# Performance work log

Measured on AMD Instinct MI355X. Metric: run time of the kernel, lower is better.

The kernel has to match this reference:

```python
import jax, jax.numpy as jnp
import numpy as np

H = 64  # hidden_size hardcoded in the module


def _lstm_scan(x_pre, w_hh):
    # x_pre: [T, B, 4H] = x @ W_ih^T + b_ih + b_hh, precomputed for all steps
    # w_hh: [4H, H]. PyTorch gate order: i, f, g, o.
    B = x_pre.shape[1]
    h0 = jnp.zeros((B, H), x_pre.dtype)
    c0 = jnp.zeros((B, H), x_pre.dtype)

    def cell(carry, xp):
        h, c = carry
        gates = xp + h @ w_hh.T  # [B, 4H]
        i, f, g, o = jnp.split(gates, 4, axis=-1)
        i = jax.nn.sigmoid(i)
        f = jax.nn.sigmoid(f)
        g = jnp.tanh(g)
        o = jax.nn.sigmoid(o)
        c = f * c + i * g
        h = o * jnp.tanh(c)
        return (h, c), h

    _, hs = jax.lax.scan(cell, (h0, c0), x_pre)
    return hs  # [T, B, H]


def _bidir_layer(x, w_ih, w_hh, b_ih, b_hh):
    # x: [T, B, D]; w_ih: [2, 4H, D]; w_hh: [2, 4H, H]; b_*: [2, 4H]
    pre_f = jnp.einsum('tbd,gd->tbg', x, w_ih[0]) + b_ih[0] + b_hh[0]
    hs_f = _lstm_scan(pre_f, w_hh[0])
    xr = x[::-1]
    pre_b = jnp.einsum('tbd,gd->tbg', xr, w_ih[1]) + b_ih[1] + b_hh[1]
    hs_b = _lstm_scan(pre_b, w_hh[1])[::-1]  # re-reverse to align with time
    return jnp.concatenate([hs_f, hs_b], axis=-1)  # [T, B, 2H]


def setup_inputs() -> dict:
    key = jax.random.key(0)
    B, T, F = 1024, 512, 32
    ks = jax.random.split(key, 11)
    s = 1.0 / float(np.sqrt(H))  # PyTorch LSTM init: U(-1/sqrt(H), 1/sqrt(H))
    u = lambda k, shape: jax.random.uniform(k, shape, jnp.float32, -s, s)
    return dict(
        x=jax.random.normal(ks[0], (B, T, F), jnp.float32),
        w_ih0=u(ks[1], (2, 4 * H, F)),
        w_hh0=u(ks[2], (2, 4 * H, H)),
        b_ih0=u(ks[3], (2, 4 * H)),
        b_hh0=u(ks[4], (2, 4 * H)),
        w_ih1=u(ks[5], (2, 4 * H, 2 * H)),
        w_hh1=u(ks[6], (2, 4 * H, H)),
        b_ih1=u(ks[7], (2, 4 * H)),
        b_hh1=u(ks[8], (2, 4 * H)),
        fc_w=u(ks[9], (2, 2 * H)),
        fc_b=u(ks[10], (2,)),
    )


def reference(x, w_ih0, w_hh0, b_ih0, b_hh0, w_ih1, w_hh1, b_ih1, b_hh1, fc_w, fc_b):
    xt = jnp.transpose(x, (1, 0, 2))  # [T, B, F]
    h1 = _bidir_layer(xt, w_ih0, w_hh0, b_ih0, b_hh0)  # [T, B, 2H]
    h2 = _bidir_layer(h1, w_ih1, w_hh1, b_ih1, b_hh1)  # [T, B, 2H]
    last = h2[-1]  # out[:, -1, :] in batch_first layout -> [B, 2H]
    return last @ fc_w.T + fc_b  # [B, 2]
```

## Files before the change

kernel.cpp:

```cpp
#include <hip/hip_runtime.h>

#define TT 512
#define BB 1024
#define FF 32
#define HH 64
#define GG 256

__device__ float g_h1[(size_t)TT * BB * 2 * HH];
__device__ float g_pre0[(size_t)2 * TT * BB * GG];
__device__ float g_pre1[(size_t)TT * BB * GG];
__device__ float g_hf[(size_t)BB * HH];

__device__ __forceinline__ float fsigm(float x) {
    float e = __builtin_amdgcn_exp2f(x * -1.44269504088896f);
    return __builtin_amdgcn_rcpf(1.0f + e);
}
__device__ __forceinline__ float ftanh(float x) {
    float e = __builtin_amdgcn_exp2f(x * -2.88539008177793f);
    return 2.0f * __builtin_amdgcn_rcpf(1.0f + e) - 1.0f;
}
__device__ __forceinline__ float rlane(float v, int l) {
    return __int_as_float(__builtin_amdgcn_readlane(__float_as_int(v), l));
}

#define FMA4(c, s, b) do { c.x += (s)*(b).x; c.y += (s)*(b).y; \
                           c.z += (s)*(b).z; c.w += (s)*(b).w; } while (0)

__global__ __launch_bounds__(256, 4) void pre_gemm0(
    const float* __restrict__ x,
    const float* __restrict__ w_ih,
    const float* __restrict__ b_ih,
    const float* __restrict__ b_hh)
{
    __shared__ __align__(16) float As[64 * 36];
    __shared__ __align__(16) float Bs[32 * 68];

    const int tid   = threadIdx.x;
    const int dir   = (int)(blockIdx.x >> 15);
    const int rem   = (int)(blockIdx.x & 32767);
    const int mt    = rem >> 2;
    const int n0    = (rem & 3) * 64;
    const int mbase = mt << 6;
    const int t     = mbase >> 10;
    const int b0    = mbase & 1023;

#pragma unroll
    for (int i = 0; i < 2; ++i) {
        const int qid = tid + 256 * i;
        const int r = qid >> 3, q = qid & 7;
        float4 v = *(const float4*)(x + ((size_t)(b0 + r) * TT + t) * FF + q * 4);
        *(float4*)(&As[r * 36 + q * 4]) = v;
    }
#pragma unroll
    for (int i = 0; i < 2; ++i) {
        const int qid = tid + 256 * i;
        const int r = qid >> 3, q = qid & 7;
        float4 v = *(const float4*)(w_ih + ((size_t)dir * GG + n0 + r) * FF + q * 4);
        Bs[(q * 4 + 0) * 68 + r] = v.x;
        Bs[(q * 4 + 1) * 68 + r] = v.y;
        Bs[(q * 4 + 2) * 68 + r] = v.z;
        Bs[(q * 4 + 3) * 68 + r] = v.w;
    }
    __syncthreads();

    const int tx = tid & 15, ty = tid >> 4;

    float4 c0 = make_float4(0.f, 0.f, 0.f, 0.f);
    float4 c1 = c0, c2 = c0, c3 = c0;

#pragma unroll
    for (int kq = 0; kq < 8; ++kq) {
        const float4 a0 = *(const float4*)&As[(ty * 4 + 0) * 36 + kq * 4];
        const float4 a1 = *(const float4*)&As[(ty * 4 + 1) * 36 + kq * 4];
        const float4 a2 = *(const float4*)&As[(ty * 4 + 2) * 36 + kq * 4];
        const float4 a3 = *(const float4*)&As[(ty * 4 + 3) * 36 + kq * 4];
        const float4 b0_ = *(const float4*)&Bs[(kq * 4 + 0) * 68 + tx * 4];
        const float4 b1_ = *(const float4*)&Bs[(kq * 4 + 1) * 68 + tx * 4];
        const float4 b2_ = *(const float4*)&Bs[(kq * 4 + 2) * 68 + tx * 4];
        const float4 b3_ = *(const float4*)&Bs[(kq * 4 + 3) * 68 + tx * 4];
        FMA4(c0, a0.x, b0_); FMA4(c0, a0.y, b1_); FMA4(c0, a0.z, b2_); FMA4(c0, a0.w, b3_);
        FMA4(c1, a1.x, b0_); FMA4(c1, a1.y, b1_); FMA4(c1, a1.z, b2_); FMA4(c1, a1.w, b3_);
        FMA4(c2, a2.x, b0_); FMA4(c2, a2.y, b1_); FMA4(c2, a2.z, b2_); FMA4(c2, a2.w, b3_);
        FMA4(c3, a3.x, b0_); FMA4(c3, a3.y, b1_); FMA4(c3, a3.z, b2_); FMA4(c3, a3.w, b3_);
    }

    float4 bias4;
    {
        const int g = dir * GG + n0 + tx * 4;
        bias4.x = b_ih[g + 0] + b_hh[g + 0];
        bias4.y = b_ih[g + 1] + b_hh[g + 1];
        bias4.z = b_ih[g + 2] + b_hh[g + 2];
        bias4.w = b_ih[g + 3] + b_hh[g + 3];
    }
    FMA4(c0, 1.f, bias4); FMA4(c1, 1.f, bias4);
    FMA4(c2, 1.f, bias4); FMA4(c3, 1.f, bias4);

    float* ob = g_pre0 +
        (((size_t)dir * TT + t) * BB + (b0 + ty * 4)) * GG + n0 + tx * 4;
    *(float4*)(ob + 0 * (size_t)GG) = c0;
    *(float4*)(ob + 1 * (size_t)GG) = c1;
    *(float4*)(ob + 2 * (size_t)GG) = c2;
    *(float4*)(ob + 3 * (size_t)GG) = c3;
}

#define PINQ(wq) \
    asm volatile("" : "+v"(wq.x), "+v"(wq.y), "+v"(wq.z), "+v"(wq.w))

template <int L>
__global__ __launch_bounds__(64, 1) void lstm_scan(
    const float* __restrict__ w_hh)
{
    const int l   = threadIdx.x;
    const int dir = (L == 0) ? (blockIdx.x & 1) : 0;
    const int b   = (L == 0) ? (int)(blockIdx.x >> 1) : (int)blockIdx.x;

    const float* wbase = w_hh + (size_t)dir * GG * HH;

    const float4* pi_ = (const float4*)(wbase + (size_t)(0  + l) * HH);
    const float4* pf_ = (const float4*)(wbase + (size_t)(64 + l) * HH);
    float4 wi0 = pi_[0],  wi1 = pi_[1],  wi2 = pi_[2],  wi3 = pi_[3],
           wi4 = pi_[4],  wi5 = pi_[5],  wi6 = pi_[6],  wi7 = pi_[7],
           wi8 = pi_[8],  wi9 = pi_[9],  wi10 = pi_[10], wi11 = pi_[11],
           wi12 = pi_[12], wi13 = pi_[13], wi14 = pi_[14], wi15 = pi_[15];
    float4 wf0 = pf_[0],  wf1 = pf_[1],  wf2 = pf_[2],  wf3 = pf_[3],
           wf4 = pf_[4],  wf5 = pf_[5],  wf6 = pf_[6],  wf7 = pf_[7],
           wf8 = pf_[8],  wf9 = pf_[9],  wf10 = pf_[10], wf11 = pf_[11],
           wf12 = pf_[12], wf13 = pf_[13], wf14 = pf_[14], wf15 = pf_[15];
    PINQ(wi0);  PINQ(wi1);  PINQ(wi2);  PINQ(wi3);
    PINQ(wi4);  PINQ(wi5);  PINQ(wi6);  PINQ(wi7);
    PINQ(wi8);  PINQ(wi9);  PINQ(wi10); PINQ(wi11);
    PINQ(wi12); PINQ(wi13); PINQ(wi14); PINQ(wi15);
    PINQ(wf0);  PINQ(wf1);  PINQ(wf2);  PINQ(wf3);
    PINQ(wf4);  PINQ(wf5);  PINQ(wf6);  PINQ(wf7);
    PINQ(wf8);  PINQ(wf9);  PINQ(wf10); PINQ(wf11);
    PINQ(wf12); PINQ(wf13); PINQ(wf14); PINQ(wf15);

    float4 wg[16], wo[16];
    {
        const float4* pg_ = (const float4*)(wbase + (size_t)(128 + l) * HH);
        const float4* po_ = (const float4*)(wbase + (size_t)(192 + l) * HH);
#pragma unroll
        for (int q = 0; q < 16; ++q) { wg[q] = pg_[q]; wo[q] = po_[q]; }
    }

    const float* pre = (L == 0) ? (g_pre0 + (size_t)dir * TT * BB * GG) : g_pre1;

    float c = 0.f, h = 0.f;

    const int t0 = dir ? (TT - 1) : 0;
    const int t1 = dir ? (TT - 2) : 1;
    const float* pp0 = pre + ((size_t)t0 * BB + b) * GG;
    const float* pp1 = pre + ((size_t)t1 * BB + b) * GG;
    float ci0 = pp0[l], cf0 = pp0[64 + l], cg0 = pp0[128 + l], co0 = pp0[192 + l];
    float ci1 = pp1[l], cf1 = pp1[64 + l], cg1 = pp1[128 + l], co1 = pp1[192 + l];

    for (int s = 0; s < TT; ++s) {
        const int t = dir ? (TT - 1 - s) : s;

        float ni = 0.f, nf = 0.f, ng = 0.f, no_ = 0.f;
        if (s + 2 < TT) {
            const int tn = dir ? (TT - 3 - s) : (s + 2);
            const float* np = pre + ((size_t)tn * BB + b) * GG;
            ni = np[l]; nf = np[64 + l]; ng = np[128 + l]; no_ = np[192 + l];
        }

        float ai = ci0, af = cf0, ag = cg0, ao = co0;

#define STEPQ(q) do {                                                        \
        float s0 = rlane(h, 4*q+0), s1 = rlane(h, 4*q+1),                    \
              s2 = rlane(h, 4*q+2), s3 = rlane(h, 4*q+3);                    \
        ai += s0*wi##q.x + s1*wi##q.y + s2*wi##q.z + s3*wi##q.w;             \
        af += s0*wf##q.x + s1*wf##q.y + s2*wf##q.z + s3*wf##q.w;             \
        ag += s0*wg[q].x + s1*wg[q].y + s2*wg[q].z + s3*wg[q].w;             \
        ao += s0*wo[q].x + s1*wo[q].y + s2*wo[q].z + s3*wo[q].w;             \
    } while (0)

        STEPQ(0);  STEPQ(1);  STEPQ(2);  STEPQ(3);
        STEPQ(4);  STEPQ(5);  STEPQ(6);  STEPQ(7);
        STEPQ(8);  STEPQ(9);  STEPQ(10); STEPQ(11);
        STEPQ(12); STEPQ(13); STEPQ(14); STEPQ(15);
#undef STEPQ

        const float ig = fsigm(ai);
        const float fg = fsigm(af);
        const float gg = ftanh(ag);
        const float og = fsigm(ao);
        c = fg * c + ig * gg;
        h = og * ftanh(c);

        if (L == 0) {
            g_h1[((size_t)t * BB + b) * (2 * HH) + dir * HH + l] = h;
        } else {
            if (s == TT - 1) g_hf[(size_t)b * HH + l] = h;
        }

        ci0 = ci1; cf0 = cf1; cg0 = cg1; co0 = co1;
        ci1 = ni;  cf1 = nf;  cg1 = ng;  co1 = no_;
    }
}

__global__ __launch_bounds__(256, 2) void pre_gemm1(
    const float* __restrict__ w_ih,
    const float* __restrict__ b_ih,
    const float* __restrict__ b_hh)
{
    __shared__ __align__(16) float As[64 * 132];
    __shared__ __align__(16) float Bs[128 * 68];

    const int tid   = threadIdx.x;
    const int mbase = (int)(blockIdx.x >> 2) * 64;
    const int n0    = (int)(blockIdx.x & 3) * 64;

#pragma unroll
    for (int i = 0; i < 8; ++i) {
        const int qid = tid + 256 * i;
        const int r = qid >> 5, q = qid & 31;
        float4 v = *(const float4*)(g_h1 + (size_t)(mbase + r) * 128 + q * 4);
        *(float4*)(&As[r * 132 + q * 4]) = v;
    }
#pragma unroll
    for (int i = 0; i < 8; ++i) {
        const int qid = tid + 256 * i;
        const int r = qid >> 5, q = qid & 31;
        float4 v = *(const float4*)(w_ih + (size_t)(n0 + r) * 128 + q * 4);
        Bs[(q * 4 + 0) * 68 + r] = v.x;
        Bs[(q * 4 + 1) * 68 + r] = v.y;
        Bs[(q * 4 + 2) * 68 + r] = v.z;
        Bs[(q * 4 + 3) * 68 + r] = v.w;
    }
    __syncthreads();

    const int tx = tid & 15, ty = tid >> 4;

    float4 c0 = make_float4(0.f, 0.f, 0.f, 0.f);
    float4 c1 = c0, c2 = c0, c3 = c0;

#pragma unroll 8
    for (int kq = 0; kq < 32; ++kq) {
        const float4 a0 = *(const float4*)&As[(ty * 4 + 0) * 132 + kq * 4];
        const float4 a1 = *(const float4*)&As[(ty * 4 + 1) * 132 + kq * 4];
        const float4 a2 = *(const float4*)&As[(ty * 4 + 2) * 132 + kq * 4];
        const float4 a3 = *(const float4*)&As[(ty * 4 + 3) * 132 + kq * 4];
        const float4 b0 = *(const float4*)&Bs[(kq * 4 + 0) * 68 + tx * 4];
        const float4 b1 = *(const float4*)&Bs[(kq * 4 + 1) * 68 + tx * 4];
        const float4 b2 = *(const float4*)&Bs[(kq * 4 + 2) * 68 + tx * 4];
        const float4 b3 = *(const float4*)&Bs[(kq * 4 + 3) * 68 + tx * 4];
        FMA4(c0, a0.x, b0); FMA4(c0, a0.y, b1); FMA4(c0, a0.z, b2); FMA4(c0, a0.w, b3);
        FMA4(c1, a1.x, b0); FMA4(c1, a1.y, b1); FMA4(c1, a1.z, b2); FMA4(c1, a1.w, b3);
        FMA4(c2, a2.x, b0); FMA4(c2, a2.y, b1); FMA4(c2, a2.z, b2); FMA4(c2, a2.w, b3);
        FMA4(c3, a3.x, b0); FMA4(c3, a3.y, b1); FMA4(c3, a3.z, b2); FMA4(c3, a3.w, b3);
    }

    float4 bias4;
    bias4.x = b_ih[n0 + tx * 4 + 0] + b_hh[n0 + tx * 4 + 0];
    bias4.y = b_ih[n0 + tx * 4 + 1] + b_hh[n0 + tx * 4 + 1];
    bias4.z = b_ih[n0 + tx * 4 + 2] + b_hh[n0 + tx * 4 + 2];
    bias4.w = b_ih[n0 + tx * 4 + 3] + b_hh[n0 + tx * 4 + 3];

    FMA4(c0, 1.f, bias4); FMA4(c1, 1.f, bias4);
    FMA4(c2, 1.f, bias4); FMA4(c3, 1.f, bias4);

    float* ob = g_pre1 + (size_t)(mbase + ty * 4) * GG + n0 + tx * 4;
    *(float4*)(ob + 0 * (size_t)GG) = c0;
    *(float4*)(ob + 1 * (size_t)GG) = c1;
    *(float4*)(ob + 2 * (size_t)GG) = c2;
    *(float4*)(ob + 3 * (size_t)GG) = c3;
}

#define FMAC4(W, P0, P1, P2, P3, K) do{                                   \
    float4 v_;                                                           \
    v_ = (P0)[K]; acc0 += W.x*v_.x; acc0 += W.y*v_.y; acc0 += W.z*v_.z; acc0 += W.w*v_.w; \
    v_ = (P1)[K]; acc1 += W.x*v_.x; acc1 += W.y*v_.y; acc1 += W.z*v_.z; acc1 += W.w*v_.w; \
    v_ = (P2)[K]; acc2 += W.x*v_.x; acc2 += W.y*v_.y; acc2 += W.z*v_.z; acc2 += W.w*v_.w; \
    v_ = (P3)[K]; acc3 += W.x*v_.x; acc3 += W.y*v_.y; acc3 += W.z*v_.z; acc3 += W.w*v_.w; \
}while(0)

__global__ __launch_bounds__(256, 2) void lstm_final(
    const float* __restrict__ w_ih,
    const float* __restrict__ b_ih,
    const float* __restrict__ b_hh,
    const float* __restrict__ fc_w,
    const float* __restrict__ fc_b,
    float* __restrict__ out)
{
    const int tid = threadIdx.x;
    const int b0  = blockIdx.x * 4;

    __shared__ __align__(16) float x_lds[4][128];
    __shared__ __align__(16) float gact[4][GG];
    __shared__ __align__(16) float last[4][128];

#pragma unroll
    for (int r = 0; r < 2; ++r) {
        int idx = tid + r * 256;
        int b = idx >> 7, col = idx & 127;
        x_lds[b][col] = g_h1[((size_t)(TT - 1) * BB + (b0 + b)) * 128 + col];
    }

    const float4* p = (const float4*)(w_ih + ((size_t)GG + tid) * 128);
    float4 w0 = p[0],  w1 = p[1],  w2 = p[2],  w3 = p[3],  w4 = p[4],  w5 = p[5],
           w6 = p[6],  w7 = p[7],  w8 = p[8],  w9 = p[9],  w10 = p[10], w11 = p[11],
           w12 = p[12], w13 = p[13], w14 = p[14], w15 = p[15], w16 = p[16], w17 = p[17],
           w18 = p[18], w19 = p[19], w20 = p[20], w21 = p[21], w22 = p[22], w23 = p[23],
           w24 = p[24], w25 = p[25], w26 = p[26], w27 = p[27], w28 = p[28], w29 = p[29],
           w30 = p[30], w31 = p[31];
    const float bias = b_ih[GG + tid] + b_hh[GG + tid];
    __syncthreads();

    const float4* xb0 = (const float4*)x_lds[0];
    const float4* xb1 = (const float4*)x_lds[1];
    const float4* xb2 = (const float4*)x_lds[2];
    const float4* xb3 = (const float4*)x_lds[3];

    float acc0 = bias, acc1 = bias, acc2 = bias, acc3 = bias;
    FMAC4(w0, xb0, xb1, xb2, xb3, 0);   FMAC4(w1, xb0, xb1, xb2, xb3, 1);
    FMAC4(w2, xb0, xb1, xb2, xb3, 2);   FMAC4(w3, xb0, xb1, xb2, xb3, 3);
    FMAC4(w4, xb0, xb1, xb2, xb3, 4);   FMAC4(w5, xb0, xb1, xb2, xb3, 5);
    FMAC4(w6, xb0, xb1, xb2, xb3, 6);   FMAC4(w7, xb0, xb1, xb2, xb3, 7);
    FMAC4(w8, xb0, xb1, xb2, xb3, 8);   FMAC4(w9, xb0, xb1, xb2, xb3, 9);
    FMAC4(w10, xb0, xb1, xb2, xb3, 10); FMAC4(w11, xb0, xb1, xb2, xb3, 11);
    FMAC4(w12, xb0, xb1, xb2, xb3, 12); FMAC4(w13, xb0, xb1, xb2, xb3, 13);
    FMAC4(w14, xb0, xb1, xb2, xb3, 14); FMAC4(w15, xb0, xb1, xb2, xb3, 15);
    FMAC4(w16, xb0, xb1, xb2, xb3, 16); FMAC4(w17, xb0, xb1, xb2, xb3, 17);
    FMAC4(w18, xb0, xb1, xb2, xb3, 18); FMAC4(w19, xb0, xb1, xb2, xb3, 19);
    FMAC4(w20, xb0, xb1, xb2, xb3, 20); FMAC4(w21, xb0, xb1, xb2, xb3, 21);
    FMAC4(w22, xb0, xb1, xb2, xb3, 22); FMAC4(w23, xb0, xb1, xb2, xb3, 23);
    FMAC4(w24, xb0, xb1, xb2, xb3, 24); FMAC4(w25, xb0, xb1, xb2, xb3, 25);
    FMAC4(w26, xb0, xb1, xb2, xb3, 26); FMAC4(w27, xb0, xb1, xb2, xb3, 27);
    FMAC4(w28, xb0, xb1, xb2, xb3, 28); FMAC4(w29, xb0, xb1, xb2, xb3, 29);
    FMAC4(w30, xb0, xb1, xb2, xb3, 30); FMAC4(w31, xb0, xb1, xb2, xb3, 31);

    const bool is_g = ((tid >> 6) == 2);
    gact[0][tid] = is_g ? ftanh(acc0) : fsigm(acc0);
    gact[1][tid] = is_g ? ftanh(acc1) : fsigm(acc1);
    gact[2][tid] = is_g ? ftanh(acc2) : fsigm(acc2);
    gact[3][tid] = is_g ? ftanh(acc3) : fsigm(acc3);
    __syncthreads();

    {
        const int cb = tid >> 6, cj = tid & 63;
        float ig = gact[cb][cj];
        float gg = gact[cb][2 * HH + cj];
        float og = gact[cb][3 * HH + cj];
        float c = ig * gg;
        float h = og * ftanh(c);
        last[cb][HH + cj] = h;
        last[cb][cj] = g_hf[(size_t)(b0 + cb) * HH + cj];
    }
    __syncthreads();

    if (tid < 8) {
        int b = tid >> 1, o = tid & 1;
        float a = fc_b[o];
#pragma unroll
        for (int j = 0; j < 128; ++j) a += fc_w[o * 128 + j] * last[b][j];
        out[(size_t)(b0 + b) * 2 + o] = a;
    }
}

extern "C" void kernel_launch(void* const* d_in, const int* in_sizes, int n_in,
                              void* d_out, int out_size, void* d_ws, size_t ws_size,
                              hipStream_t stream) {
    const float* x     = (const float*)d_in[0];
    const float* w_ih0 = (const float*)d_in[1];
    const float* w_hh0 = (const float*)d_in[2];
    const float* b_ih0 = (const float*)d_in[3];
    const float* b_hh0 = (const float*)d_in[4];
    const float* w_ih1 = (const float*)d_in[5];
    const float* w_hh1 = (const float*)d_in[6];
    const float* b_ih1 = (const float*)d_in[7];
    const float* b_hh1 = (const float*)d_in[8];
    const float* fc_w  = (const float*)d_in[9];
    const float* fc_b  = (const float*)d_in[10];
    float* out = (float*)d_out;

    pre_gemm0<<<65536, 256, 0, stream>>>(x, w_ih0, b_ih0, b_hh0);
    lstm_scan<0><<<2048, 64, 0, stream>>>(w_hh0);
    pre_gemm1<<<32768, 256, 0, stream>>>(w_ih1, b_ih1, b_hh1);
    lstm_scan<1><<<1024, 64, 0, stream>>>(w_hh1);
    lstm_final<<<256, 256, 0, stream>>>(w_ih1, b_ih1, b_hh1, fc_w, fc_b, out);
}
```

Measured before the change: 2.570 ms.

## Switch pre-activation and layer-1 hidden buffers from time-major to batch-major layout

Reorders g_pre0, g_pre1 and g_h1 from [T][B] to [B][T] indexing. The first-layer GEMM now tiles along time within one batch row, and each scan block streams its pre-activations from one contiguous region instead of jumping 1 MB per step. The goal is better DRAM/TLB locality and prefetching for the latency-bound recurrent loop. The trade-off is that per-step h1 writes across blocks are now strided in memory, and any hidden kernel that assumes time-major rows must stay consistent.

Measured after the change: 2.687 ms. 4.5% more time.

```diff
diff --git a/kernel.cpp b/kernel.cpp
--- a/kernel.cpp
+++ b/kernel.cpp
@@ -6,9 +6,9 @@
 #define HH 64
 #define GG 256
 
-__device__ float g_h1[(size_t)TT * BB * 2 * HH];
-__device__ float g_pre0[(size_t)2 * TT * BB * GG];
-__device__ float g_pre1[(size_t)TT * BB * GG];
+__device__ float g_h1[(size_t)BB * TT * 2 * HH];
+__device__ float g_pre0[(size_t)2 * BB * TT * GG];
+__device__ float g_pre1[(size_t)BB * TT * GG];
 __device__ float g_hf[(size_t)BB * HH];
 
 __device__ __forceinline__ float fsigm(float x) {
@@ -36,19 +36,19 @@
     __shared__ __align__(16) float Bs[32 * 68];
 
     const int tid   = threadIdx.x;
-    const int dir   = (int)(blockIdx.x >> 15);
-    const int rem   = (int)(blockIdx.x & 32767);
-    const int mt    = rem >> 2;
+    const int bid   = (int)blockIdx.x;
+    const int dir   = bid >> 15;
+    const int rem   = bid & 32767;
+    const int mtile = rem >> 2;
     const int n0    = (rem & 3) * 64;
-    const int mbase = mt << 6;
-    const int t     = mbase >> 10;
-    const int b0    = mbase & 1023;
+    const int b     = mtile >> 3;
+    const int t0    = (mtile & 7) << 6;
 
 #pragma unroll
     for (int i = 0; i < 2; ++i) {
         const int qid = tid + 256 * i;
         const int r = qid >> 3, q = qid & 7;
-        float4 v = *(const float4*)(x + ((size_t)(b0 + r) * TT + t) * FF + q * 4);
+        float4 v = *(const float4*)(x + ((size_t)b * TT + t0 + r) * FF + q * 4);
         *(float4*)(&As[r * 36 + q * 4]) = v;
     }
 #pragma unroll
@@ -96,7 +96,7 @@
     FMA4(c2, 1.f, bias4); FMA4(c3, 1.f, bias4);
 
     float* ob = g_pre0 +
-        (((size_t)dir * TT + t) * BB + (b0 + ty * 4)) * GG + n0 + tx * 4;
+        (((size_t)dir * BB + b) * TT + (t0 + ty * 4)) * GG + n0 + tx * 4;
     *(float4*)(ob + 0 * (size_t)GG) = c0;
     *(float4*)(ob + 1 * (size_t)GG) = c1;
     *(float4*)(ob + 2 * (size_t)GG) = c2;
@@ -143,14 +143,16 @@
         for (int q = 0; q < 16; ++q) { wg[q] = pg_[q]; wo[q] = po_[q]; }
     }
 
-    const float* pre = (L == 0) ? (g_pre0 + (size_t)dir * TT * BB * GG) : g_pre1;
+    const float* pre = (L == 0)
+        ? (g_pre0 + ((size_t)(dir * BB + b)) * TT * GG)
+        : (g_pre1 + (size_t)b * TT * GG);
 
     float c = 0.f, h = 0.f;
 
     const int t0 = dir ? (TT - 1) : 0;
     const int t1 = dir ? (TT - 2) : 1;
-    const float* pp0 = pre + ((size_t)t0 * BB + b) * GG;
-    const float* pp1 = pre + ((size_t)t1 * BB + b) * GG;
+    const float* pp0 = pre + (size_t)t0 * GG;
+    const float* pp1 = pre + (size_t)t1 * GG;
     float ci0 = pp0[l], cf0 = pp0[64 + l], cg0 = pp0[128 + l], co0 = pp0[192 + l];
     float ci1 = pp1[l], cf1 = pp1[64 + l], cg1 = pp1[128 + l], co1 = pp1[192 + l];
 
@@ -160,7 +162,7 @@
         float ni = 0.f, nf = 0.f, ng = 0.f, no_ = 0.f;
         if (s + 2 < TT) {
             const int tn = dir ? (TT - 3 - s) : (s + 2);
-            const float* np = pre + ((size_t)tn * BB + b) * GG;
+            const float* np = pre + (size_t)tn * GG;
             ni = np[l]; nf = np[64 + l]; ng = np[128 + l]; no_ = np[192 + l];
         }
 
@@ -189,7 +191,7 @@
         h = og * ftanh(c);
 
         if (L == 0) {
-            g_h1[((size_t)t * BB + b) * (2 * HH) + dir * HH + l] = h;
+            g_h1[((size_t)b * TT + t) * (2 * HH) + dir * HH + l] = h;
         } else {
             if (s == TT - 1) g_hf[(size_t)b * HH + l] = h;
         }
@@ -294,7 +296,7 @@
     for (int r = 0; r < 2; ++r) {
         int idx = tid + r * 256;
         int b = idx >> 7, col = idx & 127;
-        x_lds[b][col] = g_h1[((size_t)(TT - 1) * BB + (b0 + b)) * 128 + col];
+        x_lds[b][col] = g_h1[((size_t)(b0 + b) * TT + (TT - 1)) * 128 + col];
     }
 
     const float4* p = (const float4*)(w_ih + ((size_t)GG + tid) * 128);
```
